# Performance work log

Hardware: AMD Instinct MI355X
Metric: run time of the kernel (lower is better)

## Reference

```python
import jax, jax.numpy as jnp
import numpy as np

B, S, D = 2, 1024, 1024
E = 8          # routed experts
I = 1024       # per-expert intermediate
IS = 1024      # shared expert intermediate
TOP_K = 2
NUM_SHARED = 1


def setup_inputs() -> dict:
    key = jax.random.key(0)
    ks = jax.random.split(key, 8)
    scale = 0.02
    return {
        "x": jax.random.normal(ks[0], (B, S, D), dtype=jnp.float32),
        "w_gate": jax.random.normal(ks[1], (D, E), dtype=jnp.float32) * scale,
        "wg": jax.random.normal(ks[2], (E, D, I), dtype=jnp.float32) * scale,  # expert gate_proj
        "wu": jax.random.normal(ks[3], (E, D, I), dtype=jnp.float32) * scale,  # expert up_proj
        "wd": jax.random.normal(ks[4], (E, I, D), dtype=jnp.float32) * scale,  # expert down_proj
        "ws_g": jax.random.normal(ks[5], (NUM_SHARED, D, IS), dtype=jnp.float32) * scale,
        "ws_u": jax.random.normal(ks[6], (NUM_SHARED, D, IS), dtype=jnp.float32) * scale,
        "ws_d": jax.random.normal(ks[7], (NUM_SHARED, IS, D), dtype=jnp.float32) * scale,
    }


def _swiglu(t, w_gate_proj, w_up, w_down):
    # t: [N, D]
    g = t @ w_gate_proj            # [N, I]
    u = t @ w_up                   # [N, I]
    return (jax.nn.silu(g) * u) @ w_down  # [N, D]


def reference(x, w_gate, wg, wu, wd, ws_g, ws_u, ws_d):
    Bb, Ss, Dd = x.shape
    x_flat = x.reshape(Bb * Ss, Dd)                  # [N, D]
    N = x_flat.shape[0]

    # --- router ---
    logits = x_flat @ w_gate                          # [N, E]
    topk_logits, topk_idx = jax.lax.top_k(logits, TOP_K)
    topk_w = jax.nn.softmax(topk_logits, axis=-1)     # [N, K]

    # --- aux load-balancing loss ---
    one_hot = jax.nn.one_hot(topk_idx, E, dtype=jnp.float32)  # [N, K, E]
    f = one_hot.sum(axis=1).mean(axis=0)                       # [E]
    P = jax.nn.softmax(logits, axis=-1).mean(axis=0)           # [E]
    aux_loss = E * jnp.sum(f * P)

    # --- combine weights: cw[n, e] = sum_k topk_w[n,k] * 1[topk_idx[n,k]==e] ---
    cw = jnp.einsum("nk,nke->ne", topk_w, one_hot)             # [N, E]

    # --- routed experts: dense compute over all experts, weighted combine ---
    g = jnp.einsum("nd,edi->eni", x_flat, wg)                  # [E, N, I]
    u = jnp.einsum("nd,edi->eni", x_flat, wu)                  # [E, N, I]
    a = jax.nn.silu(g) * u                                     # [E, N, I]
    y = jnp.einsum("eni,eid->end", a, wd)                      # [E, N, D]
    routed = jnp.einsum("ne,end->nd", cw, y)                   # [N, D]

    # --- shared experts ---
    shared = jnp.zeros_like(x_flat)
    for s in range(NUM_SHARED):
        shared = shared + _swiglu(x_flat, ws_g[s], ws_u[s], ws_d[s])

    out = (routed + shared).reshape(Bb, Ss, Dd)
    return out, aux_loss
```

## Files before the change

### kernel.cpp

```cpp
#include <hip/hip_runtime.h>
#include <math.h>

typedef unsigned short u16;
typedef __attribute__((ext_vector_type(8))) short short8;
typedef __attribute__((ext_vector_type(4))) float f32x4;
typedef __attribute__((ext_vector_type(4))) unsigned short u16x4;
typedef __attribute__((ext_vector_type(8))) unsigned short u16x8;

#define N_TOK 2048
#define DIM 1024
#define OUT_ELEMS 2097152

#define GLDS16(gp, lp) __builtin_amdgcn_global_load_lds( \
    (const __attribute__((address_space(1))) unsigned int*)(gp), \
    (__attribute__((address_space(3))) unsigned int*)(lp), 16, 0, 0)

#define WAITV_N(n) do { \
    asm volatile("s_waitcnt vmcnt(" #n ")" ::: "memory"); \
    __builtin_amdgcn_sched_barrier(0); \
    __builtin_amdgcn_s_barrier(); \
    __builtin_amdgcn_sched_barrier(0); \
} while (0)

__device__ __forceinline__ u16 f2bf(float f) {
    union { float f; unsigned u; } v; v.f = f;
    unsigned r = (v.u + 0x7FFFu + ((v.u >> 16) & 1u)) >> 16;
    return (u16)r;
}
__device__ __forceinline__ float bf2f(u16 h) {
    union { unsigned u; float f; } v; v.u = ((unsigned)h) << 16;
    return v.f;
}

__device__ __forceinline__ void cvt_chunk(const float* __restrict__ src,
                                          u16* __restrict__ dst, int chunk,
                                          char* smem, int t) {
    float* tile = (float*)smem;
    const char* gsrc = (const char*)(src + (size_t)chunk * 8192);
    u16* dchunk = dst + (size_t)chunk * 8192;
    int w = t >> 6, l = t & 63;
#pragma unroll
    for (int j = 0; j < 8; j++) {
        int idx = w * 8 + j;
        GLDS16(gsrc + idx * 1024 + l * 16, smem + idx * 1024);
    }
    __syncthreads();
    int n0 = (t & 63) * 4 + (t >> 6) * 256;
    f32x4 v[8];
#pragma unroll
    for (int k = 0; k < 8; k++)
        v[k] = *(const f32x4*)(tile + k * 1024 + n0);
#pragma unroll
    for (int i = 0; i < 4; i++) {
        u16x8 o;
#pragma unroll
        for (int k = 0; k < 8; k++) o[k] = f2bf(v[k][i]);
        *(u16x8*)(dchunk + (size_t)(n0 + i) * 8) = o;
    }
}

__device__ __forceinline__ void cvt_chunk512(const float* __restrict__ src,
                                             u16* __restrict__ dst, int chunk,
                                             char* smem, int t) {
    float* tile = (float*)smem;
    const char* gsrc = (const char*)(src + (size_t)chunk * 8192);
    u16* dchunk = dst + (size_t)chunk * 8192;
    int w = t >> 6, l = t & 63;
#pragma unroll
    for (int j = 0; j < 4; j++) {
        int idx = w * 4 + j;
        GLDS16(gsrc + idx * 1024 + l * 16, smem + idx * 1024);
    }
    __syncthreads();
    int n0 = (t & 63) * 2 + (t >> 6) * 128;
    float2 v[8];
#pragma unroll
    for (int k = 0; k < 8; k++)
        v[k] = *(const float2*)(tile + k * 1024 + n0);
#pragma unroll
    for (int i = 0; i < 2; i++) {
        u16x8 o;
#pragma unroll
        for (int k = 0; k < 8; k++) o[k] = f2bf(i ? v[k].y : v[k].x);
        *(u16x8*)(dchunk + (size_t)(n0 + i) * 8) = o;
    }
}

__device__ __forceinline__ void cvt_gu_job(int j, const float* wg, const float* wu,
                                           const float* wsg, const float* wsu,
                                           u16* wgt, u16* wut, u16* wsgt, u16* wsut,
                                           char* smem, int t) {
    int mat = j >> 7, chunk = j & 127;
    const float* src; u16* dst;
    if      (mat <  8) { src = wg + (size_t)mat * 1048576;       dst = wgt + (size_t)mat * 1048576; }
    else if (mat < 16) { src = wu + (size_t)(mat - 8) * 1048576; dst = wut + (size_t)(mat - 8) * 1048576; }
    else if (mat == 16){ src = wsg; dst = wsgt; }
    else               { src = wsu; dst = wsut; }
    cvt_chunk(src, dst, chunk, smem, t);
}

__device__ __forceinline__ void cvt_d_job512(int j, const float* wd, const float* wsd,
                                             u16* wdt, u16* wsdt, char* smem, int t) {
    int mat = j >> 7, chunk = j & 127;
    const float* src = (mat < 8) ? (wd + (size_t)mat * 1048576) : wsd;
    u16* dst = (mat < 8) ? (wdt + (size_t)mat * 1048576) : wsdt;
    cvt_chunk512(src, dst, chunk, smem, t);
}

__device__ __forceinline__ void router_job(int b, const float* x, const float* wgate,
                                           u16* xb, int* tidx, float* tw,
                                           float* Pp, int* Cp, int* tlist,
                                           int* curs, char* smem, int t) {
    float* sP = (float*)smem;
    int*   sC = (int*)(smem + 64);
    if (t < 8) { sP[t] = 0.f; sC[t] = 0; }
    if (b == 0 && t < 16) curs[t] = 0;
    __syncthreads();
    int wave = t >> 6;
    int lane = t & 63;
    int n = b * 4 + wave;
    const float* xr = x + (size_t)n * DIM;
    u16* xbr = xb + (size_t)n * DIM;
    float acc[8] = {0.f,0.f,0.f,0.f,0.f,0.f,0.f,0.f};
#pragma unroll
    for (int i = 0; i < 16; i++) {
        int d = lane + i * 64;
        float xv = xr[d];
        xbr[d] = f2bf(xv);
        const float* wr = wgate + d * 8;
#pragma unroll
        for (int e = 0; e < 8; e++) acc[e] += xv * wr[e];
    }
#pragma unroll
    for (int off = 32; off; off >>= 1) {
#pragma unroll
        for (int e = 0; e < 8; e++) acc[e] += __shfl_xor(acc[e], off);
    }
    if (lane == 0) {
        tlist[4096 + n] = n;
        float mx = acc[0];
#pragma unroll
        for (int e = 1; e < 8; e++) mx = fmaxf(mx, acc[e]);
        float p[8], s = 0.f;
#pragma unroll
        for (int e = 0; e < 8; e++) { p[e] = expf(acc[e] - mx); s += p[e]; }
        float inv = 1.f / s;
#pragma unroll
        for (int e = 0; e < 8; e++) atomicAdd(&sP[e], p[e] * inv);
        int i0 = 0; float b0 = acc[0];
#pragma unroll
        for (int e = 1; e < 8; e++) if (acc[e] > b0) { b0 = acc[e]; i0 = e; }
        int i1 = -1; float b1 = -3.4e38f;
#pragma unroll
        for (int e = 0; e < 8; e++) if (e != i0 && acc[e] > b1) { b1 = acc[e]; i1 = e; }
        float w0 = 1.f / (1.f + expf(b1 - b0));
        tidx[n * 2] = i0; tidx[n * 2 + 1] = i1;
        tw[n * 2] = w0;   tw[n * 2 + 1] = 1.f - w0;
        atomicAdd(&sC[i0], 1);
        atomicAdd(&sC[i1], 1);
    }
    __syncthreads();
    if (t < 8) { Pp[b * 8 + t] = sP[t]; Cp[b * 8 + t] = sC[t]; }
}

__device__ __forceinline__ void scatter_job(int bid, const int* tidx, const float* Pp,
                                            const int* Cp, int* curs, int* tlist,
                                            int* slots, float* out, int* counts,
                                            int* offs, char* smem, int t) {
    int*   s_off = (int*)smem;
    int*   sCnt  = (int*)(smem + 32);
    float* sPs   = (float*)(smem + 64);
    int*   redC  = (int*)(smem + 128);
    float* redP  = (float*)(smem + 1152);
    int e = t & 7, g = t >> 3;
    int cs = 0; float ps = 0.f;
#pragma unroll
    for (int j = 0; j < 16; j++) {
        int b = g + j * 32;
        cs += Cp[b * 8 + e];
        ps += Pp[b * 8 + e];
    }
    redC[t] = cs; redP[t] = ps;
    __syncthreads();
    if (t < 8) {
        int c = 0; float p = 0.f;
        for (int g2 = 0; g2 < 32; g2++) { c += redC[g2 * 8 + t]; p += redP[g2 * 8 + t]; }
        sCnt[t] = c; sPs[t] = p;
    }
    __syncthreads();
    if (t == 0) {
        int o = 0;
        for (int e2 = 0; e2 < 8; e2++) { s_off[e2] = o; o += sCnt[e2]; }
    }
    __syncthreads();
    if (bid == 0 && t == 0) {
        float aux = 0.f;
        for (int e2 = 0; e2 < 8; e2++) {
            aux += (float)sCnt[e2] * sPs[e2];
            offs[e2] = s_off[e2]; counts[e2] = sCnt[e2];
        }
        out[OUT_ELEMS] = 8.f * aux / ((float)N_TOK * (float)N_TOK);
        offs[8] = 4096; counts[8] = 2048;
    }
    int n = bid * 256 + t;
    if (n < N_TOK) {
#pragma unroll
        for (int k = 0; k < 2; k++) {
            int ee = tidx[n * 2 + k];
            int p = atomicAdd(&curs[ee], 1);
            int sl = s_off[ee] + p;
            tlist[sl] = n;
            slots[n * 2 + k] = sl;
        }
    }
}

__device__ __forceinline__ void gemm_map(int jj, int& job, int& mt, int& nt) {
    if (jj < 128) { job = 8; mt = jj >> 3; nt = jj & 7; }
    else {
        int r = jj - 128;
        mt = r >> 6;
        int rem = r & 63;
        job = rem >> 3;
        nt = rem & 7;
    }
}

__device__ __forceinline__ void gemm1_job(
    int jj, const u16* __restrict__ xb, const u16* __restrict__ wgt,
    const u16* __restrict__ wut, const u16* __restrict__ wsgt,
    const u16* __restrict__ wsut, const int* __restrict__ tlist,
    const int* __restrict__ counts, const int* __restrict__ offs,
    u16* __restrict__ H, char* smem, int t) {
    int job, mt, nt; gemm_map(jj, job, mt, nt);
    int jcnt = counts[job];
    int m0 = mt << 7;
    if (m0 >= jcnt) return;
    int joff = offs[job];
    int n0 = nt << 7;
    const u16* Bg = (job < 8) ? (wgt + (size_t)job * 1048576) : wsgt;
    const u16* Bu = (job < 8) ? (wut + (size_t)job * 1048576) : wsut;

    int wave = t >> 6, lane = t & 63;
    int arow = wave * 16 + (lane >> 2);
    int tok = tlist[joff + m0 + arow];
    const u16* aA = xb + (size_t)tok * 1024 + (lane & 3) * 8;
    int cwv = wave & 3;
    const u16* pB = ((wave < 4) ? Bg : Bu) + (size_t)cwv * 8192
                  + (size_t)(n0 + lane) * 8;
    int bOff = ((wave < 4) ? 8192 : 16384) + cwv * 2048;

    int wm = (wave >> 1) << 5;
    int wn = (wave & 1) << 6;
    int quad = lane >> 4, lr = lane & 15;

    f32x4 accg[2][4], accu[2][4];
    f32x4 zz = {0.f, 0.f, 0.f, 0.f};
#pragma unroll
    for (int i = 0; i < 2; i++)
#pragma unroll
        for (int j = 0; j < 4; j++) { accg[i][j] = zz; accu[i][j] = zz; }

#define STAGE1(b_, s_) do { \
        char* bb = smem + (b_) * 24576; \
        int k0_ = (s_) * 32; \
        size_t koff_ = (size_t)k0_ * 1024; \
        GLDS16(aA + k0_, (u16*)bb + wave * 512); \
        GLDS16(pB + koff_,       (u16*)(bb + bOff)); \
        GLDS16(pB + koff_ + 512, (u16*)(bb + bOff + 1024)); \
    } while (0)

    STAGE1(0, 0);
    STAGE1(1, 1);
    WAITV_N(3);
    int cur = 0;
    for (int s = 0; s < 32; s++) {
        if (s < 30) {
            int nb = cur + 2; if (nb >= 3) nb -= 3;
            STAGE1(nb, s + 2);
        }
        const char* cb = smem + cur * 24576;
        const u16* Asr = (const u16*)cb;
        const u16* Bgr = (const u16*)(cb + 8192);
        const u16* Bur = (const u16*)(cb + 16384);
        short8 af[2], bgf[4], buf[4];
#pragma unroll
        for (int i = 0; i < 2; i++)
            af[i] = *(const short8*)(Asr + (wm + i * 16 + lr) * 32 + quad * 8);
#pragma unroll
        for (int i = 0; i < 4; i++) {
            int nrow = wn + i * 16 + lr;
            bgf[i] = *(const short8*)(Bgr + quad * 1024 + nrow * 8);
            buf[i] = *(const short8*)(Bur + quad * 1024 + nrow * 8);
        }
#pragma unroll
        for (int mi = 0; mi < 2; mi++)
#pragma unroll
            for (int ni = 0; ni < 4; ni++) {
                accg[mi][ni] = __builtin_amdgcn_mfma_f32_16x16x32_bf16(af[mi], bgf[ni], accg[mi][ni], 0, 0, 0);
                accu[mi][ni] = __builtin_amdgcn_mfma_f32_16x16x32_bf16(af[mi], buf[ni], accu[mi][ni], 0, 0, 0);
            }
        if (s < 31) {
            if (s < 30) WAITV_N(3);
            else        WAITV_N(0);
        }
        cur = cur + 1; if (cur >= 3) cur -= 3;
    }
#undef STAGE1
#pragma unroll
    for (int mi = 0; mi < 2; mi++) {
        int rowb = m0 + wm + mi * 16 + quad * 4;
#pragma unroll
        for (int rr = 0; rr < 4; rr++) {
            int row = rowb + rr;
            if (row < jcnt) {
                size_t base = (size_t)(joff + row) * 1024 + n0 + wn;
#pragma unroll
                for (int ni = 0; ni < 4; ni++) {
                    float g = accg[mi][ni][rr];
                    float u = accu[mi][ni][rr];
                    float h = (g / (1.f + expf(-g))) * u;
                    H[base + ni * 16 + lr] = f2bf(h);
                }
            }
        }
    }
}

__device__ __forceinline__ void gemm2_job(
    int jj, const u16* __restrict__ H, const u16* __restrict__ wdt,
    const u16* __restrict__ wsdt, const int* __restrict__ counts,
    const int* __restrict__ offs, u16* __restrict__ Y, char* smem, int t) {
    int job, mt, nt; gemm_map(jj, job, mt, nt);
    int jcnt = counts[job];
    int m0 = mt << 7;
    if (m0 >= jcnt) return;
    int joff = offs[job];
    int n0 = nt << 7;
    const u16* Bt = (job < 8) ? (wdt + (size_t)job * 1048576) : wsdt;

    int wave = t >> 6, lane = t & 63;
    int arow = wave * 16 + (lane >> 2);
    const u16* aA = H + (size_t)(joff + m0 + arow) * 1024 + (lane & 3) * 8;
    int cwv = wave >> 1, half = wave & 1;
    const u16* pB = Bt + (size_t)cwv * 8192 + (size_t)(n0 + half * 64 + lane) * 8;
    int bOff = 8192 + cwv * 2048 + half * 1024;

    int wm = (wave >> 1) << 5;
    int wn = (wave & 1) << 6;
    int quad = lane >> 4, lr = lane & 15;

    f32x4 acc[2][4];
    f32x4 zz = {0.f, 0.f, 0.f, 0.f};
#pragma unroll
    for (int i = 0; i < 2; i++)
#pragma unroll
        for (int j = 0; j < 4; j++) acc[i][j] = zz;

#define STAGE2(b_, s_) do { \
        char* bb = smem + (b_) * 16384; \
        int k0_ = (s_) * 32; \
        size_t koff_ = (size_t)k0_ * 1024; \
        GLDS16(aA + k0_, (u16*)bb + wave * 512); \
        GLDS16(pB + koff_, (u16*)(bb + bOff)); \
    } while (0)

    STAGE2(0, 0);
    STAGE2(1, 1);
    WAITV_N(2);
    int cur = 0;
    for (int s = 0; s < 32; s++) {
        if (s < 30) {
            int nb = cur + 2; if (nb >= 3) nb -= 3;
            STAGE2(nb, s + 2);
        }
        const char* cb = smem + cur * 16384;
        const u16* Asr = (const u16*)cb;
        const u16* Bsr = (const u16*)(cb + 8192);
        short8 af[2], bf[4];
#pragma unroll
        for (int i = 0; i < 2; i++)
            af[i] = *(const short8*)(Asr + (wm + i * 16 + lr) * 32 + quad * 8);
#pragma unroll
        for (int i = 0; i < 4; i++)
            bf[i] = *(const short8*)(Bsr + quad * 1024 + (wn + i * 16 + lr) * 8);
#pragma unroll
        for (int mi = 0; mi < 2; mi++)
#pragma unroll
            for (int ni = 0; ni < 4; ni++)
                acc[mi][ni] = __builtin_amdgcn_mfma_f32_16x16x32_bf16(af[mi], bf[ni], acc[mi][ni], 0, 0, 0);
        if (s < 31) {
            if (s < 30) WAITV_N(2);
            else        WAITV_N(0);
        }
        cur = cur + 1; if (cur >= 3) cur -= 3;
    }
#undef STAGE2
#pragma unroll
    for (int mi = 0; mi < 2; mi++) {
        int rowb = m0 + wm + mi * 16 + quad * 4;
#pragma unroll
        for (int rr = 0; rr < 4; rr++) {
            int row = rowb + rr;
            if (row < jcnt) {
                u16* yrow = Y + (size_t)(joff + row) * 1024 + n0 + wn;
#pragma unroll
                for (int ni = 0; ni < 4; ni++)
                    yrow[ni * 16 + lr] = f2bf(acc[mi][ni][rr]);
            }
        }
    }
}

__device__ __forceinline__ void combine_job(int n, const u16* __restrict__ Y,
                                            const int* __restrict__ slots,
                                            const float* __restrict__ tw,
                                            float* __restrict__ out, int t) {
    int s0 = slots[n * 2], s1 = slots[n * 2 + 1];
    float w0 = tw[n * 2], w1 = tw[n * 2 + 1];
    u16x4 y0 = ((const u16x4*)(Y + (size_t)s0 * 1024))[t];
    u16x4 y1 = ((const u16x4*)(Y + (size_t)s1 * 1024))[t];
    u16x4 ys = ((const u16x4*)(Y + (size_t)(4096 + n) * 1024))[t];
    f32x4 r;
    r.x = w0 * bf2f(y0.x) + w1 * bf2f(y1.x) + bf2f(ys.x);
    r.y = w0 * bf2f(y0.y) + w1 * bf2f(y1.y) + bf2f(ys.y);
    r.z = w0 * bf2f(y0.z) + w1 * bf2f(y1.z) + bf2f(ys.z);
    r.w = w0 * bf2f(y0.w) + w1 * bf2f(y1.w) + bf2f(ys.w);
    ((f32x4*)(out + (size_t)n * 1024))[t] = r;
}

__global__ __launch_bounds__(256)
void k_front(const float* __restrict__ wg, const float* __restrict__ wu,
             const float* __restrict__ wsg, const float* __restrict__ wsu,
             u16* __restrict__ wgt, u16* __restrict__ wut,
             u16* __restrict__ wsgt, u16* __restrict__ wsut,
             const float* __restrict__ x, const float* __restrict__ wgate,
             u16* __restrict__ xb, int* __restrict__ tidx, float* __restrict__ tw,
             float* __restrict__ Pp, int* __restrict__ Cp,
             int* __restrict__ tlist, int* __restrict__ curs) {
    __shared__ __attribute__((aligned(128))) char smem[32768];
    int bx = blockIdx.x, t = threadIdx.x;
    if (bx < 512) router_job(bx, x, wgate, xb, tidx, tw, Pp, Cp, tlist, curs, smem, t);
    else          cvt_gu_job(bx - 512, wg, wu, wsg, wsu, wgt, wut, wsgt, wsut, smem, t);
}

__global__ void k_scatter(const int* __restrict__ tidx, const float* __restrict__ Pp,
                          const int* __restrict__ Cp, int* __restrict__ curs,
                          int* __restrict__ tlist, int* __restrict__ slots,
                          float* __restrict__ out, int* __restrict__ counts,
                          int* __restrict__ offs) {
    __shared__ __attribute__((aligned(128))) char smem[4096];
    scatter_job(blockIdx.x, tidx, Pp, Cp, curs, tlist, slots, out, counts, offs,
                smem, threadIdx.x);
}

__global__ __launch_bounds__(512, 2)
void k_gemm1(const u16* __restrict__ xb, const u16* __restrict__ wgt,
             const u16* __restrict__ wut, const u16* __restrict__ wsgt,
             const u16* __restrict__ wsut, const int* __restrict__ tlist,
             const int* __restrict__ counts, const int* __restrict__ offs,
             u16* __restrict__ H,
             const float* __restrict__ wd, const float* __restrict__ wsd,
             u16* __restrict__ wdt, u16* __restrict__ wsdt) {
    __shared__ __attribute__((aligned(128))) char smem[73728];
    int bx = blockIdx.x, t = threadIdx.x;
    if (bx < 1152) gemm1_job(bx, xb, wgt, wut, wsgt, wsut, tlist, counts, offs, H, smem, t);
    else           cvt_d_job512(bx - 1152, wd, wsd, wdt, wsdt, smem, t);
}

__global__ __launch_bounds__(512, 2)
void k_gemm2(const u16* __restrict__ H, const u16* __restrict__ wdt,
             const u16* __restrict__ wsdt, const int* __restrict__ counts,
             const int* __restrict__ offs, u16* __restrict__ Y) {
    __shared__ __attribute__((aligned(128))) char smem[49152];
    gemm2_job(blockIdx.x, H, wdt, wsdt, counts, offs, Y, smem, threadIdx.x);
}

__global__ void k_combine(const u16* __restrict__ Y, const int* __restrict__ slots,
                          const float* __restrict__ tw, float* __restrict__ out) {
    combine_job(blockIdx.x, Y, slots, tw, out, threadIdx.x);
}

extern "C" void kernel_launch(void* const* d_in, const int* in_sizes, int n_in,
                              void* d_out, int out_size, void* d_ws, size_t ws_size,
                              hipStream_t stream) {
    const float* x     = (const float*)d_in[0];
    const float* wgate = (const float*)d_in[1];
    const float* wg    = (const float*)d_in[2];
    const float* wu    = (const float*)d_in[3];
    const float* wd    = (const float*)d_in[4];
    const float* wsg   = (const float*)d_in[5];
    const float* wsu   = (const float*)d_in[6];
    const float* wsd   = (const float*)d_in[7];
    float* out = (float*)d_out;

    char* ws = (char*)d_ws;
    u16*   xb    = (u16*)(ws + 0);
    u16*   wgt   = (u16*)(ws + 4194304);
    u16*   wut   = (u16*)(ws + 20971520);
    u16*   wdt   = (u16*)(ws + 37748736);
    u16*   wsgt  = (u16*)(ws + 54525952);
    u16*   wsut  = (u16*)(ws + 56623104);
    u16*   wsdt  = (u16*)(ws + 58720256);
    u16*   H     = (u16*)(ws + 60817408);
    u16*   Y     = (u16*)(ws + 4194304);
    int*   tidx  = (int*)(ws + 73400320);
    float* tw    = (float*)(ws + 73416704);
    int*   tlist = (int*)(ws + 73433088);
    int*   slots = (int*)(ws + 73457664);
    int*   counts= (int*)(ws + 73474048);
    int*   offs  = (int*)(ws + 73474112);
    int*   curs  = (int*)(ws + 73474176);
    float* Pp    = (float*)(ws + 73474304);
    int*   Cp    = (int*)(ws + 73490688);

    k_front<<<2816, 256, 0, stream>>>(wg, wu, wsg, wsu, wgt, wut, wsgt, wsut,
                                      x, wgate, xb, tidx, tw, Pp, Cp, tlist, curs);
    k_scatter<<<8, 256, 0, stream>>>(tidx, Pp, Cp, curs, tlist, slots,
                                     out, counts, offs);
    k_gemm1<<<2304, 512, 0, stream>>>(xb, wgt, wut, wsgt, wsut, tlist, counts, offs,
                                      H, wd, wsd, wdt, wsdt);
    k_gemm2<<<1152, 512, 0, stream>>>(H, wdt, wsdt, counts, offs, Y);
    k_combine<<<2048, 256, 0, stream>>>(Y, slots, tw, out);
}
```

Measured before the change: 231.4 us.

## Widen gemm2 tile to 128x256, change warp layouts, use double buffering

GEMM2 (down projection) now uses 128x256 output tiles with a 4x4 MFMA fragment grid per wave, which halves the grid to 576 blocks and cuts redundant reads of A. The pipeline moves from a 3-stage vmcnt scheme to 2-stage double buffering with __syncthreads. GEMM1 changes its wave layout from 2x4 to 4x2 fragments per wave, which alters the LDS read pattern. The trade-offs are more accumulator registers, possibly lower occupancy, and less latency hiding in GEMM2 with only two stages, plus a new job mapping.

```diff
diff --git a/kernel.cpp b/kernel.cpp
--- a/kernel.cpp
+++ b/kernel.cpp
@@ -250,16 +250,16 @@
                   + (size_t)(n0 + lane) * 8;
     int bOff = ((wave < 4) ? 8192 : 16384) + cwv * 2048;
 
-    int wm = (wave >> 1) << 5;
-    int wn = (wave & 1) << 6;
+    int wm = (wave >> 2) << 6;
+    int wn = (wave & 3) << 5;
     int quad = lane >> 4, lr = lane & 15;
 
-    f32x4 accg[2][4], accu[2][4];
+    f32x4 accg[4][2], accu[4][2];
     f32x4 zz = {0.f, 0.f, 0.f, 0.f};
 #pragma unroll
-    for (int i = 0; i < 2; i++)
-#pragma unroll
-        for (int j = 0; j < 4; j++) { accg[i][j] = zz; accu[i][j] = zz; }
+    for (int i = 0; i < 4; i++)
+#pragma unroll
+        for (int j = 0; j < 2; j++) { accg[i][j] = zz; accu[i][j] = zz; }
 
 #define STAGE1(b_, s_) do { \
         char* bb = smem + (b_) * 24576; \
@@ -283,20 +283,20 @@
         const u16* Asr = (const u16*)cb;
         const u16* Bgr = (const u16*)(cb + 8192);
         const u16* Bur = (const u16*)(cb + 16384);
-        short8 af[2], bgf[4], buf[4];
-#pragma unroll
-        for (int i = 0; i < 2; i++)
+        short8 af[4], bgf[2], buf[2];
+#pragma unroll
+        for (int i = 0; i < 4; i++)
             af[i] = *(const short8*)(Asr + (wm + i * 16 + lr) * 32 + quad * 8);
 #pragma unroll
-        for (int i = 0; i < 4; i++) {
+        for (int i = 0; i < 2; i++) {
             int nrow = wn + i * 16 + lr;
             bgf[i] = *(const short8*)(Bgr + quad * 1024 + nrow * 8);
             buf[i] = *(const short8*)(Bur + quad * 1024 + nrow * 8);
         }
 #pragma unroll
-        for (int mi = 0; mi < 2; mi++)
-#pragma unroll
-            for (int ni = 0; ni < 4; ni++) {
+        for (int mi = 0; mi < 4; mi++)
+#pragma unroll
+            for (int ni = 0; ni < 2; ni++) {
                 accg[mi][ni] = __builtin_amdgcn_mfma_f32_16x16x32_bf16(af[mi], bgf[ni], accg[mi][ni], 0, 0, 0);
                 accu[mi][ni] = __builtin_amdgcn_mfma_f32_16x16x32_bf16(af[mi], buf[ni], accu[mi][ni], 0, 0, 0);
             }
@@ -308,7 +308,7 @@
     }
 #undef STAGE1
 #pragma unroll
-    for (int mi = 0; mi < 2; mi++) {
+    for (int mi = 0; mi < 4; mi++) {
         int rowb = m0 + wm + mi * 16 + quad * 4;
 #pragma unroll
         for (int rr = 0; rr < 4; rr++) {
@@ -316,7 +316,7 @@
             if (row < jcnt) {
                 size_t base = (size_t)(joff + row) * 1024 + n0 + wn;
 #pragma unroll
-                for (int ni = 0; ni < 4; ni++) {
+                for (int ni = 0; ni < 2; ni++) {
                     float g = accg[mi][ni][rr];
                     float u = accu[mi][ni][rr];
                     float h = (g / (1.f + expf(-g))) * u;
@@ -331,73 +331,74 @@
     int jj, const u16* __restrict__ H, const u16* __restrict__ wdt,
     const u16* __restrict__ wsdt, const int* __restrict__ counts,
     const int* __restrict__ offs, u16* __restrict__ Y, char* smem, int t) {
-    int job, mt, nt; gemm_map(jj, job, mt, nt);
+    int job, mt, nt2;
+    if (jj < 64) { job = 8; mt = jj >> 2; nt2 = jj & 3; }
+    else {
+        int r = jj - 64;
+        mt = r >> 5;
+        int rem = r & 31;
+        job = rem >> 2;
+        nt2 = rem & 3;
+    }
     int jcnt = counts[job];
     int m0 = mt << 7;
     if (m0 >= jcnt) return;
     int joff = offs[job];
-    int n0 = nt << 7;
+    int n0 = nt2 << 8;
     const u16* Bt = (job < 8) ? (wdt + (size_t)job * 1048576) : wsdt;
 
     int wave = t >> 6, lane = t & 63;
     int arow = wave * 16 + (lane >> 2);
     const u16* aA = H + (size_t)(joff + m0 + arow) * 1024 + (lane & 3) * 8;
-    int cwv = wave >> 1, half = wave & 1;
-    const u16* pB = Bt + (size_t)cwv * 8192 + (size_t)(n0 + half * 64 + lane) * 8;
-    int bOff = 8192 + cwv * 2048 + half * 1024;
-
-    int wm = (wave >> 1) << 5;
-    int wn = (wave & 1) << 6;
+    int c = wave >> 1, nb = wave & 1;
+    const u16* pB = Bt + (size_t)c * 8192 + (size_t)(n0 + nb * 128 + lane) * 8;
+    int bOff = 8192 + c * 4096 + nb * 2048;
+
+    int wm = (wave >> 2) << 6;
+    int wn = (wave & 3) << 6;
     int quad = lane >> 4, lr = lane & 15;
 
-    f32x4 acc[2][4];
+    f32x4 acc[4][4];
     f32x4 zz = {0.f, 0.f, 0.f, 0.f};
 #pragma unroll
-    for (int i = 0; i < 2; i++)
+    for (int i = 0; i < 4; i++)
 #pragma unroll
         for (int j = 0; j < 4; j++) acc[i][j] = zz;
 
 #define STAGE2(b_, s_) do { \
-        char* bb = smem + (b_) * 16384; \
+        char* bb = smem + (b_) * 24576; \
         int k0_ = (s_) * 32; \
         size_t koff_ = (size_t)k0_ * 1024; \
         GLDS16(aA + k0_, (u16*)bb + wave * 512); \
-        GLDS16(pB + koff_, (u16*)(bb + bOff)); \
+        GLDS16(pB + koff_,       (u16*)(bb + bOff)); \
+        GLDS16(pB + koff_ + 512, (u16*)(bb + bOff + 1024)); \
     } while (0)
 
     STAGE2(0, 0);
-    STAGE2(1, 1);
-    WAITV_N(2);
-    int cur = 0;
+    __syncthreads();
     for (int s = 0; s < 32; s++) {
-        if (s < 30) {
-            int nb = cur + 2; if (nb >= 3) nb -= 3;
-            STAGE2(nb, s + 2);
-        }
-        const char* cb = smem + cur * 16384;
+        int cur = s & 1;
+        if (s < 31) STAGE2(cur ^ 1, s + 1);
+        const char* cb = smem + cur * 24576;
         const u16* Asr = (const u16*)cb;
         const u16* Bsr = (const u16*)(cb + 8192);
-        short8 af[2], bf[4];
-#pragma unroll
-        for (int i = 0; i < 2; i++)
+        short8 af[4], bf[4];
+#pragma unroll
+        for (int i = 0; i < 4; i++)
             af[i] = *(const short8*)(Asr + (wm + i * 16 + lr) * 32 + quad * 8);
 #pragma unroll
         for (int i = 0; i < 4; i++)
-            bf[i] = *(const short8*)(Bsr + quad * 1024 + (wn + i * 16 + lr) * 8);
-#pragma unroll
-        for (int mi = 0; mi < 2; mi++)
+            bf[i] = *(const short8*)(Bsr + quad * 2048 + (wn + i * 16 + lr) * 8);
+#pragma unroll
+        for (int mi = 0; mi < 4; mi++)
 #pragma unroll
             for (int ni = 0; ni < 4; ni++)
                 acc[mi][ni] = __builtin_amdgcn_mfma_f32_16x16x32_bf16(af[mi], bf[ni], acc[mi][ni], 0, 0, 0);
-        if (s < 31) {
-            if (s < 30) WAITV_N(2);
-            else        WAITV_N(0);
-        }
-        cur = cur + 1; if (cur >= 3) cur -= 3;
+        __syncthreads();
     }
 #undef STAGE2
 #pragma unroll
-    for (int mi = 0; mi < 2; mi++) {
+    for (int mi = 0; mi < 4; mi++) {
         int rowb = m0 + wm + mi * 16 + quad * 4;
 #pragma unroll
         for (int rr = 0; rr < 4; rr++) {
@@ -520,6 +521,6 @@
                                      out, counts, offs);
     k_gemm1<<<2304, 512, 0, stream>>>(xb, wgt, wut, wsgt, wsut, tlist, counts, offs,
                                       H, wd, wsd, wdt, wsdt);
-    k_gemm2<<<1152, 512, 0, stream>>>(H, wdt, wsdt, counts, offs, Y);
+    k_gemm2<<<576, 512, 0, stream>>>(H, wdt, wsdt, counts, offs, Y);
     k_combine<<<2048, 256, 0, stream>>>(Y, slots, tw, out);
 }
```

New measurement: 234.9 us. No clear change (+1.5%).
